# Optimization experiments

Hardware: AMD Instinct MI355X
Metric: run time of the kernel (lower is better)

## Reference

```python
import jax, jax.numpy as jnp
import numpy as np

B = 64            # batch
C = 2             # num_channels (BSF syndrome: X and Z)
L = 64            # lattice size
N = 16            # gradient (histogram) size
BIN = 360 // N    # bin_size = 22 degrees
EPS = 1e-5        # BatchNorm2d default eps


def setup_inputs() -> dict:
    key = jax.random.key(0)
    k1, = jax.random.split(key, 1)
    # syndrome in BSF: binary 0/1 values (torch.nonzero picks the set bits)
    x = jax.random.randint(k1, (B, C * L * L * L), 0, 2).astype(jnp.float32)
    gamma = jnp.ones((C,), jnp.float32)   # BatchNorm2d weight
    beta = jnp.zeros((C,), jnp.float32)   # BatchNorm2d bias
    return {"x": x, "gamma": gamma, "beta": beta}


def _bin_tables():
    # Per lattice site (i,j,k): magnitude and flattened (ax, az) bin index.
    c = jnp.arange(L, dtype=jnp.float32)
    i = c[:, None, None]
    j = c[None, :, None]
    k = c[None, None, :]
    mag = jnp.sqrt(i * i + j * j + k * k)          # (L,L,L)
    x_comp = jnp.sqrt(j * j + k * k)
    z_comp = jnp.sqrt(j * j + i * i)
    deg = 180.0 / jnp.pi
    # atan2 results are in [0, pi] here, so int() truncation == floor
    ax = jnp.floor(jnp.arctan2(x_comp, i) * deg / BIN).astype(jnp.int32)
    az = jnp.floor(jnp.arctan2(k, z_comp) * deg / BIN).astype(jnp.int32)
    bins = (ax * N + az).reshape(-1)               # (L^3,) flattened (ax,az)
    return mag.reshape(-1), bins


def reference(x, gamma, beta):
    mag, bins = _bin_tables()
    # torch.nonzero + indexed update == mask-weighted scatter of magnitudes.
    # x is 0/1, so x * mag equals the mags of the nonzero sites (0 elsewhere).
    xw = x.reshape(B, C, L * L * L) * mag                     # (B,C,L^3)
    g = jnp.zeros((B, C, N * N), x.dtype).at[:, :, bins].add(xw)
    g = g.reshape(B, C, N, N)
    # BatchNorm2d, training mode: per-channel batch statistics (biased var)
    mean = g.mean(axis=(0, 2, 3), keepdims=True)
    var = ((g - mean) ** 2).mean(axis=(0, 2, 3), keepdims=True)
    gn = (g - mean) * jax.lax.rsqrt(var + EPS)
    return gn * gamma[None, :, None, None] + beta[None, :, None, None]
```

## Files before the change

kernel.cpp:

```cpp
#include <hip/hip_runtime.h>


#define BINS_PAD 80

__global__ __launch_bounds__(256)
void bin_table_kernel(unsigned char* __restrict__ tab, float* __restrict__ g) {
    int v = blockIdx.x * 256 + threadIdx.x;
    int i = v >> 12, j = (v >> 6) & 63, k = v & 63;
    double xc2 = (double)(j * j + k * k);
    double zc2 = (double)(i * i + j * j);
    double i2  = (double)(i * i);
    double k2  = (double)(k * k);
    const double T1 = 0.4040262258351568  * 0.4040262258351568;
    const double T2 = 0.9656887748070740  * 0.9656887748070740;
    const double T3 = 2.2460367739042161  * 2.2460367739042161;
    const double T4 = 28.636253282915602  * 28.636253282915602;
    int ax = (xc2 > i2 * T1) + (xc2 > i2 * T2) + (xc2 > i2 * T3) + (xc2 > i2 * T4);
    int az = (k2 > zc2 * T1) + (k2 > zc2 * T2) + (k2 > zc2 * T3) + (k2 > zc2 * T4);
    tab[v] = (unsigned char)(ax * 16 + az);
    if (v < 32768) g[v] = 0.0f;
}

__global__ __launch_bounds__(256)
void scatter_kernel(const float4* __restrict__ x4,
                    const unsigned int* __restrict__ tabu,
                    float* __restrict__ g) {
    __shared__ float hist[4][BINS_PAD];
    int tid = threadIdx.x;
    int p   = blockIdx.x >> 4;
    int w   = tid >> 6;
    int t   = tid & 63;
    int i   = (blockIdx.x & 15) * 4 + w;
    #pragma unroll
    for (int n = tid; n < 4 * BINS_PAD; n += 256) ((float*)hist)[n] = 0.0f;
    __syncthreads();

    float* whist = hist[w];

    const float4*       xs = x4   + (size_t)p * 65536 + (size_t)i * 1024;
    const unsigned int* ts = tabu + i * 1024;

    int thi = t >> 4;
    int k0  = (t & 15) * 4;
    float kk0 = (float)(k0 * k0);
    float kk1 = (float)((k0 + 1) * (k0 + 1));
    float kk2 = (float)((k0 + 2) * (k0 + 2));
    float kk3 = (float)((k0 + 3) * (k0 + 3));
    int i2 = i * i;

    float acc = 0.0f;
    int   cur = 69;

    #pragma unroll 4
    for (int m = 0; m < 16; ++m) {
        float4       xv = xs[m * 64 + t];
        unsigned int u  = ts[m * 64 + t];
        int   j   = m * 4 + thi;
        float r2f = (float)(i2 + j * j);
        {   int b = u & 255;
            float val = xv.x * sqrtf(r2f + kk0);
            if (b != cur) { atomicAdd(&whist[cur], acc); cur = b; acc = val; }
            else          { acc += val; } }
        {   int b = (u >> 8) & 255;
            float val = xv.y * sqrtf(r2f + kk1);
            if (b != cur) { atomicAdd(&whist[cur], acc); cur = b; acc = val; }
            else          { acc += val; } }
        {   int b = (u >> 16) & 255;
            float val = xv.z * sqrtf(r2f + kk2);
            if (b != cur) { atomicAdd(&whist[cur], acc); cur = b; acc = val; }
            else          { acc += val; } }
        {   int b = (u >> 24);
            float val = xv.w * sqrtf(r2f + kk3);
            if (b != cur) { atomicAdd(&whist[cur], acc); cur = b; acc = val; }
            else          { acc += val; } }
    }
    atomicAdd(&whist[cur], acc);
    __syncthreads();

    if (tid < BINS_PAD) {
        float hv = hist[0][tid] + hist[1][tid] + hist[2][tid] + hist[3][tid];
        if (hv != 0.0f) atomicAdd(&g[p * 256 + tid], hv);
    }
}

__global__ __launch_bounds__(1024)
void norm_kernel(const float* __restrict__ g,
                 const float* __restrict__ gamma,
                 const float* __restrict__ beta,
                 float* __restrict__ out) {
    __shared__ double red[16][4];
    __shared__ float  coef[4];
    int t = threadIdx.x;
    float vals[32];
    double s0 = 0.0, s1 = 0.0, q0 = 0.0, q1 = 0.0;
    #pragma unroll
    for (int n = 0; n < 32; ++n) {
        int idx = t + n * 1024;
        float v = g[idx];
        vals[n] = v;
        double vd = (double)v;
        if ((idx >> 8) & 1) { s1 += vd; q1 += vd * vd; }
        else                { s0 += vd; q0 += vd * vd; }
    }
    #pragma unroll
    for (int off = 32; off > 0; off >>= 1) {
        s0 += __shfl_down(s0, off);
        s1 += __shfl_down(s1, off);
        q0 += __shfl_down(q0, off);
        q1 += __shfl_down(q1, off);
    }
    int wave = t >> 6;
    if ((t & 63) == 0) {
        red[wave][0] = s0; red[wave][1] = s1; red[wave][2] = q0; red[wave][3] = q1;
    }
    __syncthreads();
    if (t == 0) {
        double S0 = 0, S1 = 0, Q0 = 0, Q1 = 0;
        for (int wv = 0; wv < 16; ++wv) {
            S0 += red[wv][0]; S1 += red[wv][1]; Q0 += red[wv][2]; Q1 += red[wv][3];
        }
        const double inv_n = 1.0 / 16384.0;
        double m0 = S0 * inv_n, m1 = S1 * inv_n;
        double v0 = Q0 * inv_n - m0 * m0;
        double v1 = Q1 * inv_n - m1 * m1;
        double r0 = 1.0 / sqrt(v0 + 1e-5);
        double r1 = 1.0 / sqrt(v1 + 1e-5);
        float g0 = gamma[0], g1 = gamma[1], b0 = beta[0], b1 = beta[1];
        coef[0] = (float)r0 * g0;
        coef[1] = (float)r1 * g1;
        coef[2] = b0 - (float)(m0 * r0) * g0;
        coef[3] = b1 - (float)(m1 * r1) * g1;
    }
    __syncthreads();
    float sc0 = coef[0], sc1 = coef[1], sh0 = coef[2], sh1 = coef[3];
    #pragma unroll
    for (int n = 0; n < 32; ++n) {
        int idx = t + n * 1024;
        int c = (idx >> 8) & 1;
        out[idx] = vals[n] * (c ? sc1 : sc0) + (c ? sh1 : sh0);
    }
}

extern "C" void kernel_launch(void* const* d_in, const int* in_sizes, int n_in,
                              void* d_out, int out_size, void* d_ws, size_t ws_size,
                              hipStream_t stream) {
    const float* x     = (const float*)d_in[0];
    const float* gamma = (const float*)d_in[1];
    const float* beta  = (const float*)d_in[2];
    float* out = (float*)d_out;

    unsigned char* tab = (unsigned char*)d_ws;
    float*         g   = (float*)((char*)d_ws + 262144);

    bin_table_kernel<<<1024, 256, 0, stream>>>(tab, g);
    scatter_kernel<<<2048, 256, 0, stream>>>((const float4*)x, (const unsigned int*)tab, g);
    norm_kernel<<<1, 1024, 0, stream>>>(g, gamma, beta, out);
}
```

Baseline: 207.8 us.

## Give each scatter thread a contiguous 16-site row segment, one block per slice

The scatter kernel now launches one block per (plane, i) slice, 8192 blocks instead of 2048. Each thread owns 16 contiguous k sites of one j row and loads them as four float4s plus one uint4 of bin indices, replacing a 16-iteration strided loop. Longer contiguous runs per thread should let more same-bin values merge in registers before each shared atomic, and all loads are issued up front for memory-level parallelism. The cost is a strided per-thread access pattern (64-byte stride across lanes, poorer coalescing per instruction) and four times as many global atomics and block setups.

Result: no change. 206.6 us (-0.6%).

```diff
diff --git a/kernel.cpp b/kernel.cpp
--- a/kernel.cpp
+++ b/kernel.cpp
@@ -23,56 +23,49 @@
 
 __global__ __launch_bounds__(256)
 void scatter_kernel(const float4* __restrict__ x4,
-                    const unsigned int* __restrict__ tabu,
+                    const uint4* __restrict__ tab4,
                     float* __restrict__ g) {
     __shared__ float hist[4][BINS_PAD];
     int tid = threadIdx.x;
-    int p   = blockIdx.x >> 4;
+    int p   = blockIdx.x >> 6;
+    int i   = blockIdx.x & 63;
     int w   = tid >> 6;
-    int t   = tid & 63;
-    int i   = (blockIdx.x & 15) * 4 + w;
-    #pragma unroll
     for (int n = tid; n < 4 * BINS_PAD; n += 256) ((float*)hist)[n] = 0.0f;
     __syncthreads();
 
     float* whist = hist[w];
 
-    const float4*       xs = x4   + (size_t)p * 65536 + (size_t)i * 1024;
-    const unsigned int* ts = tabu + i * 1024;
+    int j  = tid >> 2;
+    int k0 = (tid & 3) * 16;
 
-    int thi = t >> 4;
-    int k0  = (t & 15) * 4;
-    float kk0 = (float)(k0 * k0);
-    float kk1 = (float)((k0 + 1) * (k0 + 1));
-    float kk2 = (float)((k0 + 2) * (k0 + 2));
-    float kk3 = (float)((k0 + 3) * (k0 + 3));
-    int i2 = i * i;
+    const float4* xs = x4 + (size_t)p * 65536 + (size_t)i * 1024;
+    uint4  tb  = tab4[i * 256 + tid];
+    float4 xv0 = xs[4 * tid + 0];
+    float4 xv1 = xs[4 * tid + 1];
+    float4 xv2 = xs[4 * tid + 2];
+    float4 xv3 = xs[4 * tid + 3];
+
+    float r2f = (float)(i * i + j * j);
 
     float acc = 0.0f;
     int   cur = 69;
 
-    #pragma unroll 4
-    for (int m = 0; m < 16; ++m) {
-        float4       xv = xs[m * 64 + t];
-        unsigned int u  = ts[m * 64 + t];
-        int   j   = m * 4 + thi;
-        float r2f = (float)(i2 + j * j);
-        {   int b = u & 255;
-            float val = xv.x * sqrtf(r2f + kk0);
+    float4       xq[4] = {xv0, xv1, xv2, xv3};
+    unsigned int uq[4] = {tb.x, tb.y, tb.z, tb.w};
+
+    #pragma unroll
+    for (int q = 0; q < 4; ++q) {
+        unsigned int u = uq[q];
+        float kq = (float)(k0 + q * 4);
+        #pragma unroll
+        for (int e = 0; e < 4; ++e) {
+            float k  = kq + (float)e;
+            float xe = (e == 0) ? xq[q].x : (e == 1) ? xq[q].y : (e == 2) ? xq[q].z : xq[q].w;
+            float val = xe * sqrtf(r2f + k * k);
+            int   b   = (u >> (8 * e)) & 255;
             if (b != cur) { atomicAdd(&whist[cur], acc); cur = b; acc = val; }
-            else          { acc += val; } }
-        {   int b = (u >> 8) & 255;
-            float val = xv.y * sqrtf(r2f + kk1);
-            if (b != cur) { atomicAdd(&whist[cur], acc); cur = b; acc = val; }
-            else          { acc += val; } }
-        {   int b = (u >> 16) & 255;
-            float val = xv.z * sqrtf(r2f + kk2);
-            if (b != cur) { atomicAdd(&whist[cur], acc); cur = b; acc = val; }
-            else          { acc += val; } }
-        {   int b = (u >> 24);
-            float val = xv.w * sqrtf(r2f + kk3);
-            if (b != cur) { atomicAdd(&whist[cur], acc); cur = b; acc = val; }
-            else          { acc += val; } }
+            else          { acc += val; }
+        }
     }
     atomicAdd(&whist[cur], acc);
     __syncthreads();
@@ -153,6 +146,6 @@
     float*         g   = (float*)((char*)d_ws + 262144);
 
     bin_table_kernel<<<1024, 256, 0, stream>>>(tab, g);
-    scatter_kernel<<<2048, 256, 0, stream>>>((const float4*)x, (const unsigned int*)tab, g);
+    scatter_kernel<<<8192, 256, 0, stream>>>((const float4*)x, (const uint4*)tab, g);
     norm_kernel<<<1, 1024, 0, stream>>>(g, gamma, beta, out);
 }
```
